# Kernel optimization log

Hardware: AMD Instinct MI355X
Metric: run time of the kernel (lower is better)

Reference implementation:

```python
import jax, jax.numpy as jnp
import numpy as np
import math

B, NQ, NK, D = 8, 2048, 2048, 512
EPS = 1e-8


def setup_inputs() -> dict:
    key = jax.random.key(0)
    k1, k2, k3 = jax.random.split(key, 3)
    qs = jax.random.normal(k1, (B, NQ, D), dtype=jnp.float32)
    ks = jax.random.normal(k2, (B, NK, D), dtype=jnp.float32)
    vs = jax.random.normal(k3, (B, NK, D), dtype=jnp.float32)
    scale = jnp.full((1,), math.sqrt(D), dtype=jnp.float32)  # nn.Parameter(sqrt(dim))
    bias = jnp.zeros((), dtype=jnp.float32)
    return {"qs": qs, "ks": ks, "vs": vs, "scale": scale, "bias": bias}


def _lorentz_self_inner(u):
    # <u,u>_L = -u0^2 + sum_{i>0} u_i^2 = sum u_i^2 - 2*u0^2, keepdim on last axis
    return jnp.sum(u * u, axis=-1, keepdims=True) - 2.0 * (u[..., :1] ** 2)


def reference(qs, ks, vs, scale, bias):
    # cinner: Minkowski inner product, time coord (index 0) sign-flipped on qs
    q_flip = qs.at[..., 0].multiply(-1.0)
    att = -jnp.einsum('bqd,bkd->bqk', q_flip, ks)  # -cinner(qs, ks)
    att = jax.nn.softmax(att / scale + bias, axis=-1)
    # Einstein/Lorentz midpoint: weighted sum then renormalize to the hyperboloid (k=1)
    ave = jnp.einsum('bqk,bkd->bqd', att, vs)
    denom = jnp.sqrt(jnp.clip(jnp.abs(-_lorentz_self_inner(ave)), EPS, None))
    return ave / denom
```

## Files before the change

kernel.cpp:

```cpp
#include <hip/hip_runtime.h>

#define NSEQ 2048
#define DIM  512
#define KVBLK 32
#define NKT  64
#define TILEB 32768
#define SMEMB (4 * TILEB + 4096)

typedef __bf16 bf16x8 __attribute__((ext_vector_type(8)));
typedef float  f32x4  __attribute__((ext_vector_type(4)));

__device__ __forceinline__ void gld16(const void* g, void* l) {
  __builtin_amdgcn_global_load_lds(
      (const __attribute__((address_space(1))) unsigned int*)g,
      (__attribute__((address_space(3))) unsigned int*)l, 16, 0, 0);
}

__global__ __launch_bounds__(256) void prep_k(const float* __restrict__ ks,
                                              char* __restrict__ kp) {
  int b = blockIdx.x >> 6, kt = blockIdx.x & 63;
  int t = threadIdx.x;
  const float* src = ks + ((size_t)(b * NSEQ + kt * KVBLK)) * DIM;
  char* dst = kp + ((size_t)(b * 64 + kt)) * TILEB;
#pragma unroll
  for (int i = 0; i < 8; ++i) {
    int c = t + i * 256;
    int row = c >> 6;
    int d0 = (c & 63) * 8;
    const float4* s4 = (const float4*)(src + row * DIM + d0);
    float4 x = s4[0], y = s4[1];
    bf16x8 h;
    h[0] = (__bf16)x.x; h[1] = (__bf16)x.y; h[2] = (__bf16)x.z; h[3] = (__bf16)x.w;
    h[4] = (__bf16)y.x; h[5] = (__bf16)y.y; h[6] = (__bf16)y.z; h[7] = (__bf16)y.w;
    *(bf16x8*)(dst + row * 1024 + ((d0 * 2) ^ ((row & 7) << 4))) = h;
  }
}

__global__ __launch_bounds__(256) void prep_v(const float* __restrict__ vs,
                                              char* __restrict__ vtp) {
  __shared__ __align__(16) char lds[TILEB];
  int b = blockIdx.x >> 6, kt = blockIdx.x & 63;
  int t = threadIdx.x;
  const float* src = vs + ((size_t)(b * NSEQ + kt * KVBLK)) * DIM;
#pragma unroll
  for (int i = 0; i < 8; ++i) {
    int c = t + i * 256;
    int kv = c >> 6;
    int d0 = (c & 63) * 8;
    const float4* s4 = (const float4*)(src + kv * DIM + d0);
    float4 x = s4[0], y = s4[1];
    float vals[8] = {x.x, x.y, x.z, x.w, y.x, y.y, y.z, y.w};
#pragma unroll
    for (int j = 0; j < 8; ++j) {
      int d = d0 + j;
      int byte = (d >> 1) * 128 + (((((d & 1) * 64) + kv * 2)) ^ (((d >> 1) & 7) << 4));
      *(__bf16*)(lds + byte) = (__bf16)vals[j];
    }
  }
  __syncthreads();
  char* dst = vtp + ((size_t)(b * 64 + kt)) * TILEB;
#pragma unroll
  for (int i = 0; i < 8; ++i) {
    int c16 = t + i * 256;
    *(bf16x8*)(dst + c16 * 16) = *(const bf16x8*)(lds + c16 * 16);
  }
}

__global__ __launch_bounds__(256) void attn_main(
    const float* __restrict__ qs, const char* __restrict__ kp,
    const char* __restrict__ vtp, const float* __restrict__ scale,
    float* __restrict__ out) {
  extern __shared__ __align__(16) char smem[];
  int b  = blockIdx.x & 7;
  int qt = blockIdx.x >> 3;
  int tid = threadIdx.x;
  int w = tid >> 6, lane = tid & 63;
  int c = lane & 15, g = lane >> 4;
  int q0 = qt * 64 + w * 16;

  char* kbuf = smem;
  char* vbuf = smem + 2 * TILEB;
  char* plds = smem + 4 * TILEB + w * 1024;

  float cc = 1.4426950408889634f / scale[0];

  bf16x8 qf[16];
#pragma unroll
  for (int k = 0; k < 16; ++k) {
    int d = k * 32 + g * 8;
    const float4* p = (const float4*)(qs + ((size_t)(b * NSEQ + q0 + c)) * DIM + d);
    float4 x = p[0], y = p[1];
    float vals[8] = {x.x, x.y, x.z, x.w, y.x, y.y, y.z, y.w};
    bf16x8 h;
#pragma unroll
    for (int j = 0; j < 8; ++j) {
      float mlt = (d + j == 0) ? cc : -cc;
      h[j] = (__bf16)(vals[j] * mlt);
    }
    qf[k] = h;
  }

  f32x4 acc[32];
#pragma unroll
  for (int i = 0; i < 32; ++i) acc[i] = (f32x4){0.f, 0.f, 0.f, 0.f};
  float mrow = -1e30f;

  const char* kpb = kp  + (size_t)b * 64 * TILEB;
  const char* vpb = vtp + (size_t)b * 64 * TILEB;

  const int csw = (c & 7) << 4;
  const int vt_lane = (c >> 1) * 128 +
      (((((c & 1) * 64) + g * 16)) ^ (((c >> 1) & 7) << 4));
  const int qb = (c >> 1) * 128;
  const int qh = (c & 1) * 64;
  const int qx = ((c >> 1) & 7) << 4;

#pragma unroll
  for (int i = 0; i < 8; ++i) {
    int o = tid * 16 + i * 4096;
    gld16(kpb + o, kbuf + o);
    gld16(vpb + o, vbuf + o);
    gld16(kpb + TILEB + o, kbuf + TILEB + o);
  }
  __syncthreads();

  f32x4 sl, sh;
  bf16x8 pf;

  {
    f32x4 sa0 = {0.f,0.f,0.f,0.f}, sb0 = {0.f,0.f,0.f,0.f};
    f32x4 sa1 = {0.f,0.f,0.f,0.f}, sb1 = {0.f,0.f,0.f,0.f};
    const char* krl = kbuf + c * 1024;
    const char* krh = krl + 16 * 1024;
#pragma unroll
    for (int k = 0; k < 16; ++k) {
      int bir = (k * 64 + g * 16) ^ csw;
      bf16x8 kfl = *(const bf16x8*)(krl + bir);
      bf16x8 kfh = *(const bf16x8*)(krh + bir);
      if (k & 1) {
        sb0 = __builtin_amdgcn_mfma_f32_16x16x32_bf16(kfl, qf[k], sb0, 0, 0, 0);
        sb1 = __builtin_amdgcn_mfma_f32_16x16x32_bf16(kfh, qf[k], sb1, 0, 0, 0);
      } else {
        sa0 = __builtin_amdgcn_mfma_f32_16x16x32_bf16(kfl, qf[k], sa0, 0, 0, 0);
        sa1 = __builtin_amdgcn_mfma_f32_16x16x32_bf16(kfh, qf[k], sa1, 0, 0, 0);
      }
    }
    sl = sa0 + sb0; sh = sa1 + sb1;
    float mm = fmaxf(fmaxf(fmaxf(sl[0], sl[1]), fmaxf(sl[2], sl[3])),
                     fmaxf(fmaxf(sh[0], sh[1]), fmaxf(sh[2], sh[3])));
    mm = fmaxf(mm, __shfl_xor(mm, 16));
    mm = fmaxf(mm, __shfl_xor(mm, 32));
    mrow = mm;
#pragma unroll
    for (int r = 0; r < 4; ++r) {
      float pvl = exp2f(sl[r] - mrow);
      float pvh = exp2f(sh[r] - mrow);
      int kvl = 4 * g + r;
      *(__bf16*)(plds + qb + ((qh + kvl * 2) ^ qx))        = (__bf16)pvl;
      *(__bf16*)(plds + qb + ((qh + (16 + kvl) * 2) ^ qx)) = (__bf16)pvh;
    }
    pf = *(const bf16x8*)(plds + vt_lane);
  }
  __syncthreads();

  for (int t = 0; t < NKT - 1; ++t) {
    if (t + 2 < NKT) {
      const char* ksrc = kpb + (size_t)(t + 2) * TILEB;
      char* kdst = kbuf + (t & 1) * TILEB;
#pragma unroll
      for (int i = 0; i < 8; ++i) {
        int o = tid * 16 + i * 4096;
        gld16(ksrc + o, kdst + o);
      }
    }
    {
      const char* vsrc = vpb + (size_t)(t + 1) * TILEB;
      char* vdst = vbuf + ((t + 1) & 1) * TILEB;
#pragma unroll
      for (int i = 0; i < 8; ++i) {
        int o = tid * 16 + i * 4096;
        gld16(vsrc + o, vdst + o);
      }
    }

    f32x4 sa0 = {0.f,0.f,0.f,0.f}, sb0 = {0.f,0.f,0.f,0.f};
    f32x4 sa1 = {0.f,0.f,0.f,0.f}, sb1 = {0.f,0.f,0.f,0.f};
    const char* krl = kbuf + ((t + 1) & 1) * TILEB + c * 1024;
    const char* krh = krl + 16 * 1024;
    const char* vr  = vbuf + (t & 1) * TILEB + vt_lane;
#pragma unroll
    for (int k = 0; k < 16; ++k) {
      int bir = (k * 64 + g * 16) ^ csw;
      bf16x8 kfl = *(const bf16x8*)(krl + bir);
      bf16x8 kfh = *(const bf16x8*)(krh + bir);
      bf16x8 vf0 = *(const bf16x8*)(vr + (2 * k) * 1024);
      bf16x8 vf1 = *(const bf16x8*)(vr + (2 * k + 1) * 1024);
      if (k & 1) {
        sb0 = __builtin_amdgcn_mfma_f32_16x16x32_bf16(kfl, qf[k], sb0, 0, 0, 0);
        sb1 = __builtin_amdgcn_mfma_f32_16x16x32_bf16(kfh, qf[k], sb1, 0, 0, 0);
      } else {
        sa0 = __builtin_amdgcn_mfma_f32_16x16x32_bf16(kfl, qf[k], sa0, 0, 0, 0);
        sa1 = __builtin_amdgcn_mfma_f32_16x16x32_bf16(kfh, qf[k], sa1, 0, 0, 0);
      }
      acc[2 * k]     = __builtin_amdgcn_mfma_f32_16x16x32_bf16(pf, vf0, acc[2 * k], 0, 0, 0);
      acc[2 * k + 1] = __builtin_amdgcn_mfma_f32_16x16x32_bf16(pf, vf1, acc[2 * k + 1], 0, 0, 0);
    }
    sl = sa0 + sb0; sh = sa1 + sb1;

    float mm = fmaxf(fmaxf(fmaxf(sl[0], sl[1]), fmaxf(sl[2], sl[3])),
                     fmaxf(fmaxf(sh[0], sh[1]), fmaxf(sh[2], sh[3])));
    mm = fmaxf(mm, __shfl_xor(mm, 16));
    mm = fmaxf(mm, __shfl_xor(mm, 32));
    if (__any(mm > mrow + 11.0f)) {
      float mn = fmaxf(mrow, mm);
      float f = exp2f(mrow - mn);
      mrow = mn;
      float f0 = __shfl(f, 4 * g + 0), f1 = __shfl(f, 4 * g + 1);
      float f2 = __shfl(f, 4 * g + 2), f3 = __shfl(f, 4 * g + 3);
#pragma unroll
      for (int i = 0; i < 32; ++i) {
        acc[i][0] *= f0; acc[i][1] *= f1; acc[i][2] *= f2; acc[i][3] *= f3;
      }
    }

#pragma unroll
    for (int r = 0; r < 4; ++r) {
      float pvl = exp2f(sl[r] - mrow);
      float pvh = exp2f(sh[r] - mrow);
      int kvl = 4 * g + r;
      *(__bf16*)(plds + qb + ((qh + kvl * 2) ^ qx))        = (__bf16)pvl;
      *(__bf16*)(plds + qb + ((qh + (16 + kvl) * 2) ^ qx)) = (__bf16)pvh;
    }
    pf = *(const bf16x8*)(plds + vt_lane);

    __syncthreads();
  }

  {
    const char* vr = vbuf + ((NKT - 1) & 1) * TILEB + vt_lane;
#pragma unroll
    for (int dtl = 0; dtl < 32; ++dtl) {
      bf16x8 vf = *(const bf16x8*)(vr + dtl * 1024);
      acc[dtl] = __builtin_amdgcn_mfma_f32_16x16x32_bf16(pf, vf, acc[dtl], 0, 0, 0);
    }
  }

#pragma unroll
  for (int r = 0; r < 4; ++r) {
    float ss = 0.f;
#pragma unroll
    for (int dtl = 0; dtl < 32; ++dtl) ss += acc[dtl][r] * acc[dtl][r];
    ss += __shfl_xor(ss, 1);
    ss += __shfl_xor(ss, 2);
    ss += __shfl_xor(ss, 4);
    ss += __shfl_xor(ss, 8);
    float a0 = __shfl(acc[0][r], lane & 48);
    float d2 = fabsf(2.f * a0 * a0 - ss);
    float inv = rsqrtf(fmaxf(d2, 1e-8f));
    float* orow = out + ((size_t)(b * NSEQ + q0 + 4 * g + r)) * DIM + c;
#pragma unroll
    for (int dtl = 0; dtl < 32; ++dtl) orow[dtl * 16] = acc[dtl][r] * inv;
  }
}

extern "C" void kernel_launch(void* const* d_in, const int* in_sizes, int n_in,
                              void* d_out, int out_size, void* d_ws, size_t ws_size,
                              hipStream_t stream) {
  (void)in_sizes; (void)n_in; (void)out_size;
  const float* qs = (const float*)d_in[0];
  const float* ks = (const float*)d_in[1];
  const float* vs = (const float*)d_in[2];
  const float* scale = (const float*)d_in[3];
  float* out = (float*)d_out;

  size_t need = (size_t)2 * 8 * 64 * TILEB;
  if (ws_size < need) return;
  char* kp  = (char*)d_ws;
  char* vtp = (char*)d_ws + (size_t)8 * 64 * TILEB;

  hipFuncSetAttribute((const void*)attn_main,
                      hipFuncAttributeMaxDynamicSharedMemorySize, SMEMB);

  prep_k<<<512, 256, 0, stream>>>(ks, kp);
  prep_v<<<512, 256, 0, stream>>>(vs, vtp);
  attn_main<<<256, 256, SMEMB, stream>>>(qs, kp, vtp, scale, out);
}
```

Measured before the change: 154.9 us.

## Load K fragments directly from global memory with register double-buffering, drop K LDS staging

K tiles are no longer staged through LDS with async global-to-LDS copies. Each lane now reads its swizzled K fragments straight from global memory into a two-deep register buffer that is prefetched one step ahead, and LDS usage is cut in half. The goal is to remove the K LDS traffic and its share of the barrier, and possibly to fit more blocks per CU. The risk is that every wave re-reads K from global/L2 with exposed latency that the one-step register prefetch may not hide.

```diff
diff --git a/kernel.cpp b/kernel.cpp
--- a/kernel.cpp
+++ b/kernel.cpp
@@ -5,7 +5,7 @@
 #define KVBLK 32
 #define NKT  64
 #define TILEB 32768
-#define SMEMB (4 * TILEB + 4096)
+#define SMEMB (2 * TILEB + 4096)
 
 typedef __bf16 bf16x8 __attribute__((ext_vector_type(8)));
 typedef float  f32x4  __attribute__((ext_vector_type(4)));
@@ -65,6 +65,12 @@
     *(bf16x8*)(dst + c16 * 16) = *(const bf16x8*)(lds + c16 * 16);
   }
 }
+
+#define LDK(dst, base, kk2)                                                     \
+  dst[0] = *(const bf16x8*)((base) + (((kk2) * 64 + g * 16) ^ csw));            \
+  dst[1] = *(const bf16x8*)((base) + 16384 + (((kk2) * 64 + g * 16) ^ csw));    \
+  dst[2] = *(const bf16x8*)((base) + ((((kk2) + 1) * 64 + g * 16) ^ csw));      \
+  dst[3] = *(const bf16x8*)((base) + 16384 + ((((kk2) + 1) * 64 + g * 16) ^ csw));
 
 __global__ __launch_bounds__(256) void attn_main(
     const float* __restrict__ qs, const char* __restrict__ kp,
@@ -78,9 +84,8 @@
   int c = lane & 15, g = lane >> 4;
   int q0 = qt * 64 + w * 16;
 
-  char* kbuf = smem;
-  char* vbuf = smem + 2 * TILEB;
-  char* plds = smem + 4 * TILEB + w * 1024;
+  char* vbuf = smem;
+  char* plds = smem + 2 * TILEB + w * 1024;
 
   float cc = 1.4426950408889634f / scale[0];
 
@@ -118,32 +123,25 @@
 #pragma unroll
   for (int i = 0; i < 8; ++i) {
     int o = tid * 16 + i * 4096;
-    gld16(kpb + o, kbuf + o);
     gld16(vpb + o, vbuf + o);
-    gld16(kpb + TILEB + o, kbuf + TILEB + o);
-  }
-  __syncthreads();
+  }
 
   f32x4 sl, sh;
   bf16x8 pf;
+  bf16x8 kf[2][4];
 
   {
+    const char* kt0 = kpb + c * 1024;
     f32x4 sa0 = {0.f,0.f,0.f,0.f}, sb0 = {0.f,0.f,0.f,0.f};
     f32x4 sa1 = {0.f,0.f,0.f,0.f}, sb1 = {0.f,0.f,0.f,0.f};
-    const char* krl = kbuf + c * 1024;
-    const char* krh = krl + 16 * 1024;
-#pragma unroll
-    for (int k = 0; k < 16; ++k) {
-      int bir = (k * 64 + g * 16) ^ csw;
-      bf16x8 kfl = *(const bf16x8*)(krl + bir);
-      bf16x8 kfh = *(const bf16x8*)(krh + bir);
-      if (k & 1) {
-        sb0 = __builtin_amdgcn_mfma_f32_16x16x32_bf16(kfl, qf[k], sb0, 0, 0, 0);
-        sb1 = __builtin_amdgcn_mfma_f32_16x16x32_bf16(kfh, qf[k], sb1, 0, 0, 0);
-      } else {
-        sa0 = __builtin_amdgcn_mfma_f32_16x16x32_bf16(kfl, qf[k], sa0, 0, 0, 0);
-        sa1 = __builtin_amdgcn_mfma_f32_16x16x32_bf16(kfh, qf[k], sa1, 0, 0, 0);
-      }
+    LDK(kf[0], kt0, 0)
+#pragma unroll
+    for (int kk = 0; kk < 8; ++kk) {
+      if (kk < 7) { LDK(kf[(kk + 1) & 1], kt0, 2 * kk + 2) }
+      sa0 = __builtin_amdgcn_mfma_f32_16x16x32_bf16(kf[kk & 1][0], qf[2 * kk], sa0, 0, 0, 0);
+      sa1 = __builtin_amdgcn_mfma_f32_16x16x32_bf16(kf[kk & 1][1], qf[2 * kk], sa1, 0, 0, 0);
+      sb0 = __builtin_amdgcn_mfma_f32_16x16x32_bf16(kf[kk & 1][2], qf[2 * kk + 1], sb0, 0, 0, 0);
+      sb1 = __builtin_amdgcn_mfma_f32_16x16x32_bf16(kf[kk & 1][3], qf[2 * kk + 1], sb1, 0, 0, 0);
     }
     sl = sa0 + sb0; sh = sa1 + sb1;
     float mm = fmaxf(fmaxf(fmaxf(sl[0], sl[1]), fmaxf(sl[2], sl[3])),
@@ -164,15 +162,6 @@
   __syncthreads();
 
   for (int t = 0; t < NKT - 1; ++t) {
-    if (t + 2 < NKT) {
-      const char* ksrc = kpb + (size_t)(t + 2) * TILEB;
-      char* kdst = kbuf + (t & 1) * TILEB;
-#pragma unroll
-      for (int i = 0; i < 8; ++i) {
-        int o = tid * 16 + i * 4096;
-        gld16(ksrc + o, kdst + o);
-      }
-    }
     {
       const char* vsrc = vpb + (size_t)(t + 1) * TILEB;
       char* vdst = vbuf + ((t + 1) & 1) * TILEB;
@@ -183,27 +172,27 @@
       }
     }
 
+    const char* kt1 = kpb + (size_t)(t + 1) * TILEB + c * 1024;
+    const char* vr  = vbuf + (t & 1) * TILEB + vt_lane;
+
     f32x4 sa0 = {0.f,0.f,0.f,0.f}, sb0 = {0.f,0.f,0.f,0.f};
     f32x4 sa1 = {0.f,0.f,0.f,0.f}, sb1 = {0.f,0.f,0.f,0.f};
-    const char* krl = kbuf + ((t + 1) & 1) * TILEB + c * 1024;
-    const char* krh = krl + 16 * 1024;
-    const char* vr  = vbuf + (t & 1) * TILEB + vt_lane;
-#pragma unroll
-    for (int k = 0; k < 16; ++k) {
-      int bir = (k * 64 + g * 16) ^ csw;
-      bf16x8 kfl = *(const bf16x8*)(krl + bir);
-      bf16x8 kfh = *(const bf16x8*)(krh + bir);
-      bf16x8 vf0 = *(const bf16x8*)(vr + (2 * k) * 1024);
-      bf16x8 vf1 = *(const bf16x8*)(vr + (2 * k + 1) * 1024);
-      if (k & 1) {
-        sb0 = __builtin_amdgcn_mfma_f32_16x16x32_bf16(kfl, qf[k], sb0, 0, 0, 0);
-        sb1 = __builtin_amdgcn_mfma_f32_16x16x32_bf16(kfh, qf[k], sb1, 0, 0, 0);
-      } else {
-        sa0 = __builtin_amdgcn_mfma_f32_16x16x32_bf16(kfl, qf[k], sa0, 0, 0, 0);
-        sa1 = __builtin_amdgcn_mfma_f32_16x16x32_bf16(kfh, qf[k], sa1, 0, 0, 0);
-      }
-      acc[2 * k]     = __builtin_amdgcn_mfma_f32_16x16x32_bf16(pf, vf0, acc[2 * k], 0, 0, 0);
-      acc[2 * k + 1] = __builtin_amdgcn_mfma_f32_16x16x32_bf16(pf, vf1, acc[2 * k + 1], 0, 0, 0);
+    LDK(kf[0], kt1, 0)
+#pragma unroll
+    for (int kk = 0; kk < 8; ++kk) {
+      if (kk < 7) { LDK(kf[(kk + 1) & 1], kt1, 2 * kk + 2) }
+      bf16x8 vf0 = *(const bf16x8*)(vr + (4 * kk + 0) * 1024);
+      bf16x8 vf1 = *(const bf16x8*)(vr + (4 * kk + 1) * 1024);
+      bf16x8 vf2 = *(const bf16x8*)(vr + (4 * kk + 2) * 1024);
+      bf16x8 vf3 = *(const bf16x8*)(vr + (4 * kk + 3) * 1024);
+      acc[4 * kk + 0] = __builtin_amdgcn_mfma_f32_16x16x32_bf16(pf, vf0, acc[4 * kk + 0], 0, 0, 0);
+      acc[4 * kk + 1] = __builtin_amdgcn_mfma_f32_16x16x32_bf16(pf, vf1, acc[4 * kk + 1], 0, 0, 0);
+      acc[4 * kk + 2] = __builtin_amdgcn_mfma_f32_16x16x32_bf16(pf, vf2, acc[4 * kk + 2], 0, 0, 0);
+      acc[4 * kk + 3] = __builtin_amdgcn_mfma_f32_16x16x32_bf16(pf, vf3, acc[4 * kk + 3], 0, 0, 0);
+      sa0 = __builtin_amdgcn_mfma_f32_16x16x32_bf16(kf[kk & 1][0], qf[2 * kk], sa0, 0, 0, 0);
+      sa1 = __builtin_amdgcn_mfma_f32_16x16x32_bf16(kf[kk & 1][1], qf[2 * kk], sa1, 0, 0, 0);
+      sb0 = __builtin_amdgcn_mfma_f32_16x16x32_bf16(kf[kk & 1][2], qf[2 * kk + 1], sb0, 0, 0, 0);
+      sb1 = __builtin_amdgcn_mfma_f32_16x16x32_bf16(kf[kk & 1][3], qf[2 * kk + 1], sb1, 0, 0, 0);
     }
     sl = sa0 + sb0; sh = sa1 + sb1;
 
```

Result: slower. 238.1 us (+53.7%).

## Split KV range across wave pairs with two query groups per wave

Applied to the files above, without the earlier changes.

Adds a new attention kernel in which each wave handles two 16-row query groups, so every K and V fragment read from LDS feeds twice as many MFMAs. The four waves are split into two KV halves that run independent online softmax and are merged at the end through LDS. The kernel asks for one wave per EU so that it has enough registers for the doubled accumulators. It runs only when the compiled kernel shows no scratch spilling, and otherwise falls back to the old kernel. The cost is much higher register pressure, a final cross-wave merge, and dropping the old overlap of QK with PV within each iteration.

```diff
diff --git a/kernel.cpp b/kernel.cpp
--- a/kernel.cpp
+++ b/kernel.cpp
@@ -4,8 +4,10 @@
 #define DIM  512
 #define KVBLK 32
 #define NKT  64
+#define NIT  32
 #define TILEB 32768
-#define SMEMB (4 * TILEB + 4096)
+#define SMEMB_A (4 * TILEB + 8192)
+#define SMEMB_4 (4 * TILEB + 4096)
 
 typedef __bf16 bf16x8 __attribute__((ext_vector_type(8)));
 typedef float  f32x4  __attribute__((ext_vector_type(4)));
@@ -66,7 +68,215 @@
   }
 }
 
-__global__ __launch_bounds__(256) void attn_main(
+#define MFMA __builtin_amdgcn_mfma_f32_16x16x32_bf16
+
+__global__
+__attribute__((amdgpu_flat_work_group_size(256, 256)))
+__attribute__((amdgpu_waves_per_eu(1, 1)))
+void attn_mainA(const float* __restrict__ qs, const char* __restrict__ kp,
+                const char* __restrict__ vtp, const float* __restrict__ scale,
+                float* __restrict__ out) {
+  extern __shared__ __align__(16) char smem[];
+  int b  = blockIdx.x & 7;
+  int qt = blockIdx.x >> 3;
+  int tid = threadIdx.x;
+  int w = tid >> 6, lane = tid & 63;
+  int qs2 = w & 1, kvh = w >> 1;
+  int c = lane & 15, g = lane >> 4;
+  int q0 = qt * 64 + qs2 * 32;
+
+  char* kbuf = smem + kvh * TILEB;
+  char* vbuf = smem + 2 * TILEB + kvh * TILEB;
+  char* plds = smem + 4 * TILEB + w * 2048;
+
+  float cc = 1.4426950408889634f / scale[0];
+
+  bf16x8 qfA[16], qfB[16];
+#pragma unroll
+  for (int k = 0; k < 16; ++k) {
+    int d = k * 32 + g * 8;
+#pragma unroll
+    for (int grp = 0; grp < 2; ++grp) {
+      int row = q0 + grp * 16 + c;
+      const float4* p = (const float4*)(qs + ((size_t)(b * NSEQ + row)) * DIM + d);
+      float4 x = p[0], y = p[1];
+      float vals[8] = {x.x, x.y, x.z, x.w, y.x, y.y, y.z, y.w};
+      bf16x8 h;
+#pragma unroll
+      for (int j = 0; j < 8; ++j) {
+        float mlt = (d + j == 0) ? cc : -cc;
+        h[j] = (__bf16)(vals[j] * mlt);
+      }
+      if (grp == 0) qfA[k] = h; else qfB[k] = h;
+    }
+  }
+
+  f32x4 accA[32], accB[32];
+#pragma unroll
+  for (int i = 0; i < 32; ++i) { accA[i] = (f32x4){0,0,0,0}; accB[i] = (f32x4){0,0,0,0}; }
+  float mrowA = -1e30f, mrowB = -1e30f;
+
+  const char* kS0 = kp  + (size_t)b * 64 * TILEB;
+  const char* kS1 = kS0 + (size_t)32 * TILEB;
+  const char* vS0 = vtp + (size_t)b * 64 * TILEB;
+  const char* vS1 = vS0 + (size_t)32 * TILEB;
+
+  const int csw = (c & 7) << 4;
+  const int vt_lane = (c >> 1) * 128 +
+      (((((c & 1) * 64) + g * 16)) ^ (((c >> 1) & 7) << 4));
+  const int qb = (c >> 1) * 128;
+  const int qh = (c & 1) * 64;
+  const int qx = ((c >> 1) & 7) << 4;
+
+#pragma unroll
+  for (int i = 0; i < 8; ++i) {
+    int o = tid * 16 + i * 4096;
+    gld16(kS0 + o, smem + o);
+    gld16(kS1 + o, smem + TILEB + o);
+    gld16(vS0 + o, smem + 2 * TILEB + o);
+    gld16(vS1 + o, smem + 3 * TILEB + o);
+  }
+  __syncthreads();
+
+  const char* krl = kbuf + c * 1024;
+  const char* vr  = vbuf + vt_lane;
+
+  for (int t = 0; t < NIT; ++t) {
+    f32x4 sAl = {0,0,0,0}, sAh = {0,0,0,0}, sBl = {0,0,0,0}, sBh = {0,0,0,0};
+#pragma unroll
+    for (int k = 0; k < 16; ++k) {
+      int bir = (k * 64 + g * 16) ^ csw;
+      bf16x8 kfl = *(const bf16x8*)(krl + bir);
+      bf16x8 kfh = *(const bf16x8*)(krl + 16384 + bir);
+      sAl = MFMA(kfl, qfA[k], sAl, 0, 0, 0);
+      sBl = MFMA(kfl, qfB[k], sBl, 0, 0, 0);
+      sAh = MFMA(kfh, qfA[k], sAh, 0, 0, 0);
+      sBh = MFMA(kfh, qfB[k], sBh, 0, 0, 0);
+    }
+    __syncthreads();
+    if (t + 1 < NIT) {
+      size_t off = (size_t)(t + 1) * TILEB;
+#pragma unroll
+      for (int i = 0; i < 8; ++i) {
+        int o = tid * 16 + i * 4096;
+        gld16(kS0 + off + o, smem + o);
+        gld16(kS1 + off + o, smem + TILEB + o);
+      }
+    }
+
+    float mmA = fmaxf(fmaxf(fmaxf(sAl[0], sAl[1]), fmaxf(sAl[2], sAl[3])),
+                      fmaxf(fmaxf(sAh[0], sAh[1]), fmaxf(sAh[2], sAh[3])));
+    float mmB = fmaxf(fmaxf(fmaxf(sBl[0], sBl[1]), fmaxf(sBl[2], sBl[3])),
+                      fmaxf(fmaxf(sBh[0], sBh[1]), fmaxf(sBh[2], sBh[3])));
+    mmA = fmaxf(mmA, __shfl_xor(mmA, 16)); mmA = fmaxf(mmA, __shfl_xor(mmA, 32));
+    mmB = fmaxf(mmB, __shfl_xor(mmB, 16)); mmB = fmaxf(mmB, __shfl_xor(mmB, 32));
+    bool grow = (mmA > mrowA + 11.0f) || (mmB > mrowB + 11.0f);
+    if (__any(grow)) {
+      float MA = fmaxf(mrowA, mmA), MB = fmaxf(mrowB, mmB);
+      float fA = exp2f(mrowA - MA), fB = exp2f(mrowB - MB);
+      mrowA = MA; mrowB = MB;
+      float fA0 = __shfl(fA, 4*g+0), fA1 = __shfl(fA, 4*g+1);
+      float fA2 = __shfl(fA, 4*g+2), fA3 = __shfl(fA, 4*g+3);
+      float fB0 = __shfl(fB, 4*g+0), fB1 = __shfl(fB, 4*g+1);
+      float fB2 = __shfl(fB, 4*g+2), fB3 = __shfl(fB, 4*g+3);
+#pragma unroll
+      for (int i = 0; i < 32; ++i) {
+        accA[i][0] *= fA0; accA[i][1] *= fA1; accA[i][2] *= fA2; accA[i][3] *= fA3;
+        accB[i][0] *= fB0; accB[i][1] *= fB1; accB[i][2] *= fB2; accB[i][3] *= fB3;
+      }
+    }
+#pragma unroll
+    for (int r = 0; r < 4; ++r) {
+      int kvl = 4 * g + r;
+      float pAl = exp2f(sAl[r] - mrowA), pAh = exp2f(sAh[r] - mrowA);
+      float pBl = exp2f(sBl[r] - mrowB), pBh = exp2f(sBh[r] - mrowB);
+      *(__bf16*)(plds + qb + ((qh + kvl * 2) ^ qx))               = (__bf16)pAl;
+      *(__bf16*)(plds + qb + ((qh + (16 + kvl) * 2) ^ qx))        = (__bf16)pAh;
+      *(__bf16*)(plds + 1024 + qb + ((qh + kvl * 2) ^ qx))        = (__bf16)pBl;
+      *(__bf16*)(plds + 1024 + qb + ((qh + (16 + kvl) * 2) ^ qx)) = (__bf16)pBh;
+    }
+    bf16x8 pfA = *(const bf16x8*)(plds + vt_lane);
+    bf16x8 pfB = *(const bf16x8*)(plds + 1024 + vt_lane);
+
+#pragma unroll
+    for (int dtl = 0; dtl < 32; ++dtl) {
+      bf16x8 vf = *(const bf16x8*)(vr + dtl * 1024);
+      accA[dtl] = MFMA(pfA, vf, accA[dtl], 0, 0, 0);
+      accB[dtl] = MFMA(pfB, vf, accB[dtl], 0, 0, 0);
+    }
+    __syncthreads();
+    if (t + 1 < NIT) {
+      size_t off = (size_t)(t + 1) * TILEB;
+#pragma unroll
+      for (int i = 0; i < 8; ++i) {
+        int o = tid * 16 + i * 4096;
+        gld16(vS0 + off + o, smem + 2 * TILEB + o);
+        gld16(vS1 + off + o, smem + 3 * TILEB + o);
+      }
+    }
+  }
+
+  if (g == 0) {
+    *(float*)(plds + c * 4)      = mrowA;
+    *(float*)(plds + 64 + c * 4) = mrowB;
+  }
+  __syncthreads();
+  {
+    const char* pp = smem + 4 * TILEB + ((1 - kvh) * 2 + qs2) * 2048;
+    float mpA = *(const float*)(pp + c * 4);
+    float mpB = *(const float*)(pp + 64 + c * 4);
+    float fA = exp2f(mrowA - fmaxf(mrowA, mpA));
+    float fB = exp2f(mrowB - fmaxf(mrowB, mpB));
+    float fA0 = __shfl(fA, 4*g+0), fA1 = __shfl(fA, 4*g+1);
+    float fA2 = __shfl(fA, 4*g+2), fA3 = __shfl(fA, 4*g+3);
+    float fB0 = __shfl(fB, 4*g+0), fB1 = __shfl(fB, 4*g+1);
+    float fB2 = __shfl(fB, 4*g+2), fB3 = __shfl(fB, 4*g+3);
+#pragma unroll
+    for (int i = 0; i < 32; ++i) {
+      accA[i][0] *= fA0; accA[i][1] *= fA1; accA[i][2] *= fA2; accA[i][3] *= fA3;
+      accB[i][0] *= fB0; accB[i][1] *= fB1; accB[i][2] *= fB2; accB[i][3] *= fB3;
+    }
+  }
+  if (kvh == 1) {
+    char* mg = smem + qs2 * 65536;
+#pragma unroll
+    for (int i = 0; i < 32; ++i) *(f32x4*)(mg + i * 1024 + lane * 16) = accA[i];
+#pragma unroll
+    for (int i = 0; i < 32; ++i) *(f32x4*)(mg + 32768 + i * 1024 + lane * 16) = accB[i];
+  }
+  __syncthreads();
+  if (kvh == 0) {
+    const char* mg = smem + qs2 * 65536;
+#pragma unroll
+    for (int i = 0; i < 32; ++i) accA[i] += *(const f32x4*)(mg + i * 1024 + lane * 16);
+#pragma unroll
+    for (int i = 0; i < 32; ++i) accB[i] += *(const f32x4*)(mg + 32768 + i * 1024 + lane * 16);
+
+#pragma unroll
+    for (int grp = 0; grp < 2; ++grp) {
+      f32x4* acc = grp ? accB : accA;
+      int qg = q0 + grp * 16;
+#pragma unroll
+      for (int r = 0; r < 4; ++r) {
+        float ss = 0.f;
+#pragma unroll
+        for (int dtl = 0; dtl < 32; ++dtl) ss += acc[dtl][r] * acc[dtl][r];
+        ss += __shfl_xor(ss, 1);
+        ss += __shfl_xor(ss, 2);
+        ss += __shfl_xor(ss, 4);
+        ss += __shfl_xor(ss, 8);
+        float a0 = __shfl(acc[0][r], lane & 48);
+        float d2 = fabsf(2.f * a0 * a0 - ss);
+        float inv = rsqrtf(fmaxf(d2, 1e-8f));
+        float* orow = out + ((size_t)(b * NSEQ + qg + 4 * g + r)) * DIM + c;
+#pragma unroll
+        for (int dtl = 0; dtl < 32; ++dtl) orow[dtl * 16] = acc[dtl][r] * inv;
+      }
+    }
+  }
+}
+
+__global__ __launch_bounds__(256) void attn_main4(
     const float* __restrict__ qs, const char* __restrict__ kp,
     const char* __restrict__ vtp, const float* __restrict__ scale,
     float* __restrict__ out) {
@@ -126,10 +336,8 @@
 
   f32x4 sl, sh;
   bf16x8 pf;
-
   {
-    f32x4 sa0 = {0.f,0.f,0.f,0.f}, sb0 = {0.f,0.f,0.f,0.f};
-    f32x4 sa1 = {0.f,0.f,0.f,0.f}, sb1 = {0.f,0.f,0.f,0.f};
+    f32x4 sa0 = {0,0,0,0}, sb0 = {0,0,0,0}, sa1 = {0,0,0,0}, sb1 = {0,0,0,0};
     const char* krl = kbuf + c * 1024;
     const char* krh = krl + 16 * 1024;
 #pragma unroll
@@ -138,11 +346,11 @@
       bf16x8 kfl = *(const bf16x8*)(krl + bir);
       bf16x8 kfh = *(const bf16x8*)(krh + bir);
       if (k & 1) {
-        sb0 = __builtin_amdgcn_mfma_f32_16x16x32_bf16(kfl, qf[k], sb0, 0, 0, 0);
-        sb1 = __builtin_amdgcn_mfma_f32_16x16x32_bf16(kfh, qf[k], sb1, 0, 0, 0);
+        sb0 = MFMA(kfl, qf[k], sb0, 0, 0, 0);
+        sb1 = MFMA(kfh, qf[k], sb1, 0, 0, 0);
       } else {
-        sa0 = __builtin_amdgcn_mfma_f32_16x16x32_bf16(kfl, qf[k], sa0, 0, 0, 0);
-        sa1 = __builtin_amdgcn_mfma_f32_16x16x32_bf16(kfh, qf[k], sa1, 0, 0, 0);
+        sa0 = MFMA(kfl, qf[k], sa0, 0, 0, 0);
+        sa1 = MFMA(kfh, qf[k], sa1, 0, 0, 0);
       }
     }
     sl = sa0 + sb0; sh = sa1 + sb1;
@@ -182,9 +390,7 @@
         gld16(vsrc + o, vdst + o);
       }
     }
-
-    f32x4 sa0 = {0.f,0.f,0.f,0.f}, sb0 = {0.f,0.f,0.f,0.f};
-    f32x4 sa1 = {0.f,0.f,0.f,0.f}, sb1 = {0.f,0.f,0.f,0.f};
+    f32x4 sa0 = {0,0,0,0}, sb0 = {0,0,0,0}, sa1 = {0,0,0,0}, sb1 = {0,0,0,0};
     const char* krl = kbuf + ((t + 1) & 1) * TILEB + c * 1024;
     const char* krh = krl + 16 * 1024;
     const char* vr  = vbuf + (t & 1) * TILEB + vt_lane;
@@ -196,14 +402,14 @@
       bf16x8 vf0 = *(const bf16x8*)(vr + (2 * k) * 1024);
       bf16x8 vf1 = *(const bf16x8*)(vr + (2 * k + 1) * 1024);
       if (k & 1) {
-        sb0 = __builtin_amdgcn_mfma_f32_16x16x32_bf16(kfl, qf[k], sb0, 0, 0, 0);
-        sb1 = __builtin_amdgcn_mfma_f32_16x16x32_bf16(kfh, qf[k], sb1, 0, 0, 0);
+        sb0 = MFMA(kfl, qf[k], sb0, 0, 0, 0);
+        sb1 = MFMA(kfh, qf[k], sb1, 0, 0, 0);
       } else {
-        sa0 = __builtin_amdgcn_mfma_f32_16x16x32_bf16(kfl, qf[k], sa0, 0, 0, 0);
-        sa1 = __builtin_amdgcn_mfma_f32_16x16x32_bf16(kfh, qf[k], sa1, 0, 0, 0);
-      }
-      acc[2 * k]     = __builtin_amdgcn_mfma_f32_16x16x32_bf16(pf, vf0, acc[2 * k], 0, 0, 0);
-      acc[2 * k + 1] = __builtin_amdgcn_mfma_f32_16x16x32_bf16(pf, vf1, acc[2 * k + 1], 0, 0, 0);
+        sa0 = MFMA(kfl, qf[k], sa0, 0, 0, 0);
+        sa1 = MFMA(kfh, qf[k], sa1, 0, 0, 0);
+      }
+      acc[2 * k]     = MFMA(pf, vf0, acc[2 * k], 0, 0, 0);
+      acc[2 * k + 1] = MFMA(pf, vf1, acc[2 * k + 1], 0, 0, 0);
     }
     sl = sa0 + sb0; sh = sa1 + sb1;
 
@@ -222,7 +428,6 @@
         acc[i][0] *= f0; acc[i][1] *= f1; acc[i][2] *= f2; acc[i][3] *= f3;
       }
     }
-
 #pragma unroll
     for (int r = 0; r < 4; ++r) {
       float pvl = exp2f(sl[r] - mrow);
@@ -232,19 +437,16 @@
       *(__bf16*)(plds + qb + ((qh + (16 + kvl) * 2) ^ qx)) = (__bf16)pvh;
     }
     pf = *(const bf16x8*)(plds + vt_lane);
-
     __syncthreads();
   }
-
   {
     const char* vr = vbuf + ((NKT - 1) & 1) * TILEB + vt_lane;
 #pragma unroll
     for (int dtl = 0; dtl < 32; ++dtl) {
       bf16x8 vf = *(const bf16x8*)(vr + dtl * 1024);
-      acc[dtl] = __builtin_amdgcn_mfma_f32_16x16x32_bf16(pf, vf, acc[dtl], 0, 0, 0);
-    }
-  }
-
+      acc[dtl] = MFMA(pf, vf, acc[dtl], 0, 0, 0);
+    }
+  }
 #pragma unroll
   for (int r = 0; r < 4; ++r) {
     float ss = 0.f;
@@ -278,10 +480,21 @@
   char* kp  = (char*)d_ws;
   char* vtp = (char*)d_ws + (size_t)8 * 64 * TILEB;
 
-  hipFuncSetAttribute((const void*)attn_main,
-                      hipFuncAttributeMaxDynamicSharedMemorySize, SMEMB);
-
   prep_k<<<512, 256, 0, stream>>>(ks, kp);
   prep_v<<<512, 256, 0, stream>>>(vs, vtp);
-  attn_main<<<256, 256, SMEMB, stream>>>(qs, kp, vtp, scale, out);
+
+  hipFuncAttributes aA;
+  bool useA = false;
+  if (hipFuncGetAttributes(&aA, (const void*)attn_mainA) == hipSuccess)
+    useA = (aA.localSizeBytes == 0);
+
+  if (useA) {
+    hipFuncSetAttribute((const void*)attn_mainA,
+                        hipFuncAttributeMaxDynamicSharedMemorySize, SMEMB_A);
+    attn_mainA<<<256, 256, SMEMB_A, stream>>>(qs, kp, vtp, scale, out);
+  } else {
+    hipFuncSetAttribute((const void*)attn_main4,
+                        hipFuncAttributeMaxDynamicSharedMemorySize, SMEMB_4);
+    attn_main4<<<256, 256, SMEMB_4, stream>>>(qs, kp, vtp, scale, out);
+  }
 }
```

Result: no change. 154.9 us (-0.0%).

## Split attention into producer waves for QK/softmax and consumer waves for PV

Applied to the files above, without the earlier changes.

Adds a 384-thread warp-specialized attention kernel. Two producer waves each compute QK^T scores and softmax probabilities for 32 query rows. Four consumer waves accumulate P·V, each owning half of the output dimension. Probabilities and rescale factors pass through double-buffered LDS. The aim is to overlap score computation with PV accumulation across waves and to halve per-wave accumulator registers. The cost is extra LDS traffic and a runtime fallback to the old kernel when register or spill attributes look wrong.

```diff
diff --git a/kernel.cpp b/kernel.cpp
--- a/kernel.cpp
+++ b/kernel.cpp
@@ -2,10 +2,13 @@
 
 #define NSEQ 2048
 #define DIM  512
-#define KVBLK 32
 #define NKT  64
 #define TILEB 32768
-#define SMEMB (4 * TILEB + 4096)
+#define VOFF  65536
+#define POFF  131072
+#define FOFF  139264
+#define SMEMB 139776
+#define SMEMB4 (4 * TILEB + 4096)
 
 typedef __bf16 bf16x8 __attribute__((ext_vector_type(8)));
 typedef float  f32x4  __attribute__((ext_vector_type(4)));
@@ -16,11 +19,13 @@
       (__attribute__((address_space(3))) unsigned int*)l, 16, 0, 0);
 }
 
+#define MFMA __builtin_amdgcn_mfma_f32_16x16x32_bf16
+
 __global__ __launch_bounds__(256) void prep_k(const float* __restrict__ ks,
                                               char* __restrict__ kp) {
   int b = blockIdx.x >> 6, kt = blockIdx.x & 63;
   int t = threadIdx.x;
-  const float* src = ks + ((size_t)(b * NSEQ + kt * KVBLK)) * DIM;
+  const float* src = ks + ((size_t)(b * NSEQ + kt * 32)) * DIM;
   char* dst = kp + ((size_t)(b * 64 + kt)) * TILEB;
 #pragma unroll
   for (int i = 0; i < 8; ++i) {
@@ -41,7 +46,7 @@
   __shared__ __align__(16) char lds[TILEB];
   int b = blockIdx.x >> 6, kt = blockIdx.x & 63;
   int t = threadIdx.x;
-  const float* src = vs + ((size_t)(b * NSEQ + kt * KVBLK)) * DIM;
+  const float* src = vs + ((size_t)(b * NSEQ + kt * 32)) * DIM;
 #pragma unroll
   for (int i = 0; i < 8; ++i) {
     int c = t + i * 256;
@@ -51,10 +56,10 @@
     float4 x = s4[0], y = s4[1];
     float vals[8] = {x.x, x.y, x.z, x.w, y.x, y.y, y.z, y.w};
 #pragma unroll
-    for (int j = 0; j < 8; ++j) {
-      int d = d0 + j;
+    for (int jj = 0; jj < 8; ++jj) {
+      int d = d0 + jj;
       int byte = (d >> 1) * 128 + (((((d & 1) * 64) + kv * 2)) ^ (((d >> 1) & 7) << 4));
-      *(__bf16*)(lds + byte) = (__bf16)vals[j];
+      *(__bf16*)(lds + byte) = (__bf16)vals[jj];
     }
   }
   __syncthreads();
@@ -66,7 +71,232 @@
   }
 }
 
-__global__ __launch_bounds__(256) void attn_main(
+__global__ __launch_bounds__(384, 1) void attn_pc(
+    const float* __restrict__ qs, const char* __restrict__ kp,
+    const char* __restrict__ vtp, const float* __restrict__ scale,
+    float* __restrict__ out) {
+  extern __shared__ __align__(16) char smem[];
+  int b  = blockIdx.x & 7;
+  int qt = blockIdx.x >> 3;
+  int tid = threadIdx.x;
+  int w = tid >> 6, lane = tid & 63;
+  int c = lane & 15, g = lane >> 4;
+  const bool prod = (w < 2);
+  const int u = prod ? w : ((w - 2) >> 1);
+  const int j = (w - 2) & 1;
+  const int q0 = qt * 64 + u * 32;
+
+  const char* kpb = kp  + (size_t)b * 64 * TILEB;
+  const char* vpb = vtp + (size_t)b * 64 * TILEB;
+
+  const int csw = (c & 7) << 4;
+  const int vt_lane = (c >> 1) * 128 +
+      (((((c & 1) * 64) + g * 16)) ^ (((c >> 1) & 7) << 4));
+  const int qb = (c >> 1) * 128;
+  const int qh = (c & 1) * 64;
+  const int qx = ((c >> 1) & 7) << 4;
+
+  float cc = 1.4426950408889634f / scale[0];
+
+  f32x4 st[32];
+  float mrowA = -1e30f, mrowB = -1e30f;
+
+  if (prod) {
+#pragma unroll
+    for (int k = 0; k < 16; ++k) {
+      int d = k * 32 + g * 8;
+#pragma unroll
+      for (int grp = 0; grp < 2; ++grp) {
+        int row = q0 + grp * 16 + c;
+        const float4* p = (const float4*)(qs + ((size_t)(b * NSEQ + row)) * DIM + d);
+        float4 x = p[0], y = p[1];
+        float vals[8] = {x.x, x.y, x.z, x.w, y.x, y.y, y.z, y.w};
+        bf16x8 h;
+#pragma unroll
+        for (int jj = 0; jj < 8; ++jj) {
+          float mlt = (d + jj == 0) ? cc : -cc;
+          h[jj] = (__bf16)(vals[jj] * mlt);
+        }
+        st[grp * 16 + k] = __builtin_bit_cast(f32x4, h);
+      }
+    }
+  } else {
+#pragma unroll
+    for (int i = 0; i < 32; ++i) st[i] = (f32x4){0.f, 0.f, 0.f, 0.f};
+  }
+
+  auto STAGE = [&](const char* src, char* dst) {
+#pragma unroll
+    for (int i = 0; i < 6; ++i) {
+      int o = tid * 16 + i * 6144;
+      if (o < TILEB) gld16(src + o, dst + o);
+    }
+  };
+
+  auto PRODUCE = [&](int tile, int par, bool first) {
+    f32x4 a0A={0,0,0,0}, a1A={0,0,0,0}, b0A={0,0,0,0}, b1A={0,0,0,0};
+    f32x4 a0B={0,0,0,0}, a1B={0,0,0,0}, b0B={0,0,0,0}, b1B={0,0,0,0};
+    const char* krl = smem + (tile & 1) * TILEB + c * 1024;
+    const char* krh = krl + 16 * 1024;
+#pragma unroll
+    for (int k = 0; k < 16; ++k) {
+      int bir = (k * 64 + g * 16) ^ csw;
+      bf16x8 kfl = *(const bf16x8*)(krl + bir);
+      bf16x8 kfh = *(const bf16x8*)(krh + bir);
+      bf16x8 qA = __builtin_bit_cast(bf16x8, st[k]);
+      bf16x8 qB = __builtin_bit_cast(bf16x8, st[16 + k]);
+      if (k & 1) {
+        b0A = MFMA(kfl, qA, b0A, 0,0,0); b1A = MFMA(kfh, qA, b1A, 0,0,0);
+        b0B = MFMA(kfl, qB, b0B, 0,0,0); b1B = MFMA(kfh, qB, b1B, 0,0,0);
+      } else {
+        a0A = MFMA(kfl, qA, a0A, 0,0,0); a1A = MFMA(kfh, qA, a1A, 0,0,0);
+        a0B = MFMA(kfl, qB, a0B, 0,0,0); a1B = MFMA(kfh, qB, a1B, 0,0,0);
+      }
+    }
+    f32x4 slA = a0A + b0A, shA = a1A + b1A;
+    f32x4 slB = a0B + b0B, shB = a1B + b1B;
+    float mmA = fmaxf(fmaxf(fmaxf(slA[0], slA[1]), fmaxf(slA[2], slA[3])),
+                      fmaxf(fmaxf(shA[0], shA[1]), fmaxf(shA[2], shA[3])));
+    float mmB = fmaxf(fmaxf(fmaxf(slB[0], slB[1]), fmaxf(slB[2], slB[3])),
+                      fmaxf(fmaxf(shB[0], shB[1]), fmaxf(shB[2], shB[3])));
+    mmA = fmaxf(mmA, __shfl_xor(mmA, 16)); mmA = fmaxf(mmA, __shfl_xor(mmA, 32));
+    mmB = fmaxf(mmB, __shfl_xor(mmB, 16)); mmB = fmaxf(mmB, __shfl_xor(mmB, 32));
+    float fA = 1.0f, fB = 1.0f;
+    if (first) {
+      mrowA = mmA; mrowB = mmB;
+    } else if (__any((mmA > mrowA + 11.0f) || (mmB > mrowB + 11.0f))) {
+      float MA = fmaxf(mrowA, mmA), MB = fmaxf(mrowB, mmB);
+      fA = exp2f(mrowA - MA); fB = exp2f(mrowB - MB);
+      mrowA = MA; mrowB = MB;
+    }
+    char* fb = smem + FOFF + par * 256 + u * 128;
+    if (g == 0) {
+      *(float*)(fb + c * 4)      = fA;
+      *(float*)(fb + 64 + c * 4) = fB;
+    }
+    char* pbA = smem + POFF + par * 4096 + u * 2048;
+    char* pbB = pbA + 1024;
+#pragma unroll
+    for (int r = 0; r < 4; ++r) {
+      int kvl = 4 * g + r;
+      float pAl = exp2f(slA[r] - mrowA), pAh = exp2f(shA[r] - mrowA);
+      float pBl = exp2f(slB[r] - mrowB), pBh = exp2f(shB[r] - mrowB);
+      *(__bf16*)(pbA + qb + ((qh + kvl * 2) ^ qx))        = (__bf16)pAl;
+      *(__bf16*)(pbA + qb + ((qh + (16 + kvl) * 2) ^ qx)) = (__bf16)pAh;
+      *(__bf16*)(pbB + qb + ((qh + kvl * 2) ^ qx))        = (__bf16)pBl;
+      *(__bf16*)(pbB + qb + ((qh + (16 + kvl) * 2) ^ qx)) = (__bf16)pBh;
+    }
+  };
+
+  auto CONSUME = [&](int t) {
+    int par = t & 1;
+    const char* fb = smem + FOFF + par * 256 + u * 128;
+    float fvA = *(const float*)(fb + c * 4);
+    float fvB = *(const float*)(fb + 64 + c * 4);
+    if (__any((fvA < 1.0f) || (fvB < 1.0f))) {
+      float fA0 = __shfl(fvA, 4*g+0), fA1 = __shfl(fvA, 4*g+1);
+      float fA2 = __shfl(fvA, 4*g+2), fA3 = __shfl(fvA, 4*g+3);
+      float fB0 = __shfl(fvB, 4*g+0), fB1 = __shfl(fvB, 4*g+1);
+      float fB2 = __shfl(fvB, 4*g+2), fB3 = __shfl(fvB, 4*g+3);
+#pragma unroll
+      for (int i = 0; i < 16; ++i) {
+        st[i][0] *= fA0; st[i][1] *= fA1; st[i][2] *= fA2; st[i][3] *= fA3;
+        st[16+i][0] *= fB0; st[16+i][1] *= fB1; st[16+i][2] *= fB2; st[16+i][3] *= fB3;
+      }
+    }
+    const char* pbA = smem + POFF + par * 4096 + u * 2048;
+    bf16x8 pfA = *(const bf16x8*)(pbA + vt_lane);
+    bf16x8 pfB = *(const bf16x8*)(pbA + 1024 + vt_lane);
+    const char* vr = smem + VOFF + par * TILEB + j * 16384 + vt_lane;
+#pragma unroll
+    for (int dtl = 0; dtl < 16; ++dtl) {
+      bf16x8 vf = *(const bf16x8*)(vr + dtl * 1024);
+      st[dtl]      = MFMA(pfA, vf, st[dtl], 0, 0, 0);
+      st[16 + dtl] = MFMA(pfB, vf, st[16 + dtl], 0, 0, 0);
+    }
+  };
+
+  STAGE(kpb, smem);
+  STAGE(kpb + TILEB, smem + TILEB);
+  STAGE(vpb, smem + VOFF);
+  __syncthreads();
+  if (prod) PRODUCE(0, 0, true);
+  __syncthreads();
+
+  for (int t = 0; t < NKT; ++t) {
+    if (t + 2 < NKT) STAGE(kpb + (size_t)(t + 2) * TILEB, smem + (t & 1) * TILEB);
+    if (t + 1 < NKT) STAGE(vpb + (size_t)(t + 1) * TILEB, smem + VOFF + ((t + 1) & 1) * TILEB);
+    if (prod) {
+      if (t + 1 < NKT) PRODUCE(t + 1, (t + 1) & 1, false);
+    } else {
+      CONSUME(t);
+    }
+    __syncthreads();
+  }
+
+  char* mrg = smem + POFF + u * 512;
+  float ssA[4], ssB[4];
+  if (!prod) {
+#pragma unroll
+    for (int r = 0; r < 4; ++r) {
+      float sA = 0.f, sB = 0.f;
+#pragma unroll
+      for (int i = 0; i < 16; ++i) {
+        sA += st[i][r] * st[i][r];
+        sB += st[16 + i][r] * st[16 + i][r];
+      }
+      sA += __shfl_xor(sA, 1); sA += __shfl_xor(sA, 2);
+      sA += __shfl_xor(sA, 4); sA += __shfl_xor(sA, 8);
+      sB += __shfl_xor(sB, 1); sB += __shfl_xor(sB, 2);
+      sB += __shfl_xor(sB, 4); sB += __shfl_xor(sB, 8);
+      ssA[r] = sA; ssB[r] = sB;
+    }
+    if (j == 1 && c == 0) {
+#pragma unroll
+      for (int r = 0; r < 4; ++r) {
+        *(float*)(mrg + (4 * g + r) * 4)      = ssA[r];
+        *(float*)(mrg + 64 + (4 * g + r) * 4) = ssB[r];
+      }
+    }
+  }
+  __syncthreads();
+  if (!prod && j == 0) {
+#pragma unroll
+    for (int grp = 0; grp < 2; ++grp) {
+#pragma unroll
+      for (int r = 0; r < 4; ++r) {
+        float sown = grp ? ssB[r] : ssA[r];
+        float soth = *(const float*)(mrg + grp * 64 + (4 * g + r) * 4);
+        float ss = sown + soth;
+        f32x4 acc0 = grp ? st[16] : st[0];
+        float a0 = __shfl(acc0[r], lane & 48);
+        float d2 = fabsf(2.f * a0 * a0 - ss);
+        float inv = rsqrtf(fmaxf(d2, 1e-8f));
+        if (c == 0) *(float*)(mrg + 128 + grp * 64 + (4 * g + r) * 4) = inv;
+        float* orow = out + ((size_t)(b * NSEQ + q0 + grp * 16 + 4 * g + r)) * DIM + c;
+#pragma unroll
+        for (int i = 0; i < 16; ++i)
+          orow[i * 16] = (grp ? st[16 + i][r] : st[i][r]) * inv;
+      }
+    }
+  }
+  __syncthreads();
+  if (!prod && j == 1) {
+#pragma unroll
+    for (int grp = 0; grp < 2; ++grp) {
+#pragma unroll
+      for (int r = 0; r < 4; ++r) {
+        float inv = *(const float*)(mrg + 128 + grp * 64 + (4 * g + r) * 4);
+        float* orow = out + ((size_t)(b * NSEQ + q0 + grp * 16 + 4 * g + r)) * DIM + 256 + c;
+#pragma unroll
+        for (int i = 0; i < 16; ++i)
+          orow[i * 16] = (grp ? st[16 + i][r] : st[i][r]) * inv;
+      }
+    }
+  }
+}
+
+__global__ __launch_bounds__(256) void attn_main4(
     const float* __restrict__ qs, const char* __restrict__ kp,
     const char* __restrict__ vtp, const float* __restrict__ scale,
     float* __restrict__ out) {
@@ -93,9 +323,9 @@
     float vals[8] = {x.x, x.y, x.z, x.w, y.x, y.y, y.z, y.w};
     bf16x8 h;
 #pragma unroll
-    for (int j = 0; j < 8; ++j) {
-      float mlt = (d + j == 0) ? cc : -cc;
-      h[j] = (__bf16)(vals[j] * mlt);
+    for (int jj = 0; jj < 8; ++jj) {
+      float mlt = (d + jj == 0) ? cc : -cc;
+      h[jj] = (__bf16)(vals[jj] * mlt);
     }
     qf[k] = h;
   }
@@ -126,10 +356,8 @@
 
   f32x4 sl, sh;
   bf16x8 pf;
-
   {
-    f32x4 sa0 = {0.f,0.f,0.f,0.f}, sb0 = {0.f,0.f,0.f,0.f};
-    f32x4 sa1 = {0.f,0.f,0.f,0.f}, sb1 = {0.f,0.f,0.f,0.f};
+    f32x4 sa0 = {0,0,0,0}, sb0 = {0,0,0,0}, sa1 = {0,0,0,0}, sb1 = {0,0,0,0};
     const char* krl = kbuf + c * 1024;
     const char* krh = krl + 16 * 1024;
 #pragma unroll
@@ -137,13 +365,8 @@
       int bir = (k * 64 + g * 16) ^ csw;
       bf16x8 kfl = *(const bf16x8*)(krl + bir);
       bf16x8 kfh = *(const bf16x8*)(krh + bir);
-      if (k & 1) {
-        sb0 = __builtin_amdgcn_mfma_f32_16x16x32_bf16(kfl, qf[k], sb0, 0, 0, 0);
-        sb1 = __builtin_amdgcn_mfma_f32_16x16x32_bf16(kfh, qf[k], sb1, 0, 0, 0);
-      } else {
-        sa0 = __builtin_amdgcn_mfma_f32_16x16x32_bf16(kfl, qf[k], sa0, 0, 0, 0);
-        sa1 = __builtin_amdgcn_mfma_f32_16x16x32_bf16(kfh, qf[k], sa1, 0, 0, 0);
-      }
+      if (k & 1) { sb0 = MFMA(kfl, qf[k], sb0, 0,0,0); sb1 = MFMA(kfh, qf[k], sb1, 0,0,0); }
+      else       { sa0 = MFMA(kfl, qf[k], sa0, 0,0,0); sa1 = MFMA(kfh, qf[k], sa1, 0,0,0); }
     }
     sl = sa0 + sb0; sh = sa1 + sb1;
     float mm = fmaxf(fmaxf(fmaxf(sl[0], sl[1]), fmaxf(sl[2], sl[3])),
@@ -182,9 +405,7 @@
         gld16(vsrc + o, vdst + o);
       }
     }
-
-    f32x4 sa0 = {0.f,0.f,0.f,0.f}, sb0 = {0.f,0.f,0.f,0.f};
-    f32x4 sa1 = {0.f,0.f,0.f,0.f}, sb1 = {0.f,0.f,0.f,0.f};
+    f32x4 sa0 = {0,0,0,0}, sb0 = {0,0,0,0}, sa1 = {0,0,0,0}, sb1 = {0,0,0,0};
     const char* krl = kbuf + ((t + 1) & 1) * TILEB + c * 1024;
     const char* krh = krl + 16 * 1024;
     const char* vr  = vbuf + (t & 1) * TILEB + vt_lane;
@@ -195,15 +416,10 @@
       bf16x8 kfh = *(const bf16x8*)(krh + bir);
       bf16x8 vf0 = *(const bf16x8*)(vr + (2 * k) * 1024);
       bf16x8 vf1 = *(const bf16x8*)(vr + (2 * k + 1) * 1024);
-      if (k & 1) {
-        sb0 = __builtin_amdgcn_mfma_f32_16x16x32_bf16(kfl, qf[k], sb0, 0, 0, 0);
-        sb1 = __builtin_amdgcn_mfma_f32_16x16x32_bf16(kfh, qf[k], sb1, 0, 0, 0);
-      } else {
-        sa0 = __builtin_amdgcn_mfma_f32_16x16x32_bf16(kfl, qf[k], sa0, 0, 0, 0);
-        sa1 = __builtin_amdgcn_mfma_f32_16x16x32_bf16(kfh, qf[k], sa1, 0, 0, 0);
-      }
-      acc[2 * k]     = __builtin_amdgcn_mfma_f32_16x16x32_bf16(pf, vf0, acc[2 * k], 0, 0, 0);
-      acc[2 * k + 1] = __builtin_amdgcn_mfma_f32_16x16x32_bf16(pf, vf1, acc[2 * k + 1], 0, 0, 0);
+      if (k & 1) { sb0 = MFMA(kfl, qf[k], sb0, 0,0,0); sb1 = MFMA(kfh, qf[k], sb1, 0,0,0); }
+      else       { sa0 = MFMA(kfl, qf[k], sa0, 0,0,0); sa1 = MFMA(kfh, qf[k], sa1, 0,0,0); }
+      acc[2 * k]     = MFMA(pf, vf0, acc[2 * k], 0, 0, 0);
+      acc[2 * k + 1] = MFMA(pf, vf1, acc[2 * k + 1], 0, 0, 0);
     }
     sl = sa0 + sb0; sh = sa1 + sb1;
 
@@ -222,7 +438,6 @@
         acc[i][0] *= f0; acc[i][1] *= f1; acc[i][2] *= f2; acc[i][3] *= f3;
       }
     }
-
 #pragma unroll
     for (int r = 0; r < 4; ++r) {
       float pvl = exp2f(sl[r] - mrow);
@@ -232,19 +447,16 @@
       *(__bf16*)(plds + qb + ((qh + (16 + kvl) * 2) ^ qx)) = (__bf16)pvh;
     }
     pf = *(const bf16x8*)(plds + vt_lane);
-
     __syncthreads();
   }
-
   {
     const char* vr = vbuf + ((NKT - 1) & 1) * TILEB + vt_lane;
 #pragma unroll
     for (int dtl = 0; dtl < 32; ++dtl) {
       bf16x8 vf = *(const bf16x8*)(vr + dtl * 1024);
-      acc[dtl] = __builtin_amdgcn_mfma_f32_16x16x32_bf16(pf, vf, acc[dtl], 0, 0, 0);
-    }
-  }
-
+      acc[dtl] = MFMA(pf, vf, acc[dtl], 0, 0, 0);
+    }
+  }
 #pragma unroll
   for (int r = 0; r < 4; ++r) {
     float ss = 0.f;
@@ -278,10 +490,21 @@
   char* kp  = (char*)d_ws;
   char* vtp = (char*)d_ws + (size_t)8 * 64 * TILEB;
 
-  hipFuncSetAttribute((const void*)attn_main,
-                      hipFuncAttributeMaxDynamicSharedMemorySize, SMEMB);
-
   prep_k<<<512, 256, 0, stream>>>(ks, kp);
   prep_v<<<512, 256, 0, stream>>>(vs, vtp);
-  attn_main<<<256, 256, SMEMB, stream>>>(qs, kp, vtp, scale, out);
+
+  hipFuncAttributes a;
+  bool usePC = false;
+  if (hipFuncGetAttributes(&a, (const void*)attn_pc) == hipSuccess)
+    usePC = (a.localSizeBytes == 0 && a.numRegs >= 100);
+
+  if (usePC) {
+    hipFuncSetAttribute((const void*)attn_pc,
+                        hipFuncAttributeMaxDynamicSharedMemorySize, SMEMB);
+    attn_pc<<<256, 384, SMEMB, stream>>>(qs, kp, vtp, scale, out);
+  } else {
+    hipFuncSetAttribute((const void*)attn_main4,
+                        hipFuncAttributeMaxDynamicSharedMemorySize, SMEMB4);
+    attn_main4<<<256, 256, SMEMB4, stream>>>(qs, kp, vtp, scale, out);
+  }
 }
```

Result: no change. 157.3 us (+1.5%).
